# Kernel tuning notes

Measured on AMD Instinct MI355X. Metric: run time of the kernel, lower is better.

The kernel has to match this reference:

```python
import jax, jax.numpy as jnp
import numpy as np

NUM_EMBEDDINGS = 4096
EMBEDDING_DIM = 256
COMMITMENT_COST = 0.25


def setup_inputs() -> dict:
    key = jax.random.key(0)
    k1, k2 = jax.random.split(key)
    x = jax.random.normal(k1, (64, 32, 32, EMBEDDING_DIM), dtype=jnp.float32)
    # torch init: uniform(-1/K, 1/K)
    codebook = jax.random.uniform(
        k2, (NUM_EMBEDDINGS, EMBEDDING_DIM), dtype=jnp.float32,
        minval=-1.0 / NUM_EMBEDDINGS, maxval=1.0 / NUM_EMBEDDINGS)
    return {"x": x, "codebook": codebook}


def reference(x, codebook):
    D = codebook.shape[1]
    flat_x = x.reshape(-1, D)                                   # [N, D]
    distances = (jnp.sum(flat_x ** 2, axis=1, keepdims=True)
                 + jnp.sum(codebook ** 2, axis=1)
                 - 2.0 * flat_x @ codebook.T)                   # [N, K]
    encoding_indices = jnp.argmin(distances, axis=1)            # [N]
    quantized = codebook[encoding_indices].reshape(x.shape)     # gather (== one-hot matmul)
    q_sg = jax.lax.stop_gradient(quantized)
    x_sg = jax.lax.stop_gradient(x)
    commitment_loss = jnp.mean((q_sg - x) ** 2)
    codebook_loss = jnp.mean((quantized - x_sg) ** 2)
    vq_loss = codebook_loss + COMMITMENT_COST * commitment_loss
    # straight-through estimator
    quantized_st = x + jax.lax.stop_gradient(quantized - x)
    return quantized_st, vq_loss
```

## Files before the change

kernel.cpp:

```cpp
#include <hip/hip_runtime.h>
#include <stdint.h>

#define DIM     256
#define NCODES  4096
#define NROWS   65536
#define ROWS_WG 128
#define CCOLS   64
#define NCH     (NCODES / CCOLS)
#define CHB     (CCOLS * DIM)

#define OFF_BIMG  0u
#define OFF_HC    (1u << 20)
#define OFF_PART  ((1u << 20) + 16384u)

typedef __attribute__((ext_vector_type(8)))  int   i32x8;
typedef __attribute__((ext_vector_type(16))) float f32x16;
typedef const __attribute__((address_space(1))) uint32_t* gas1_t;
typedef __attribute__((address_space(3))) uint32_t*       las3_t;

__device__ __forceinline__ uint32_t pk4(float a, float b, float c, float d) {
  uint32_t lo = (uint32_t)__builtin_amdgcn_cvt_pk_fp8_f32(a, b, 0, false) & 0xFFFFu;
  uint32_t hi = (uint32_t)__builtin_amdgcn_cvt_pk_fp8_f32(c, d, 0, false) & 0xFFFFu;
  return lo | (hi << 16);
}

__global__ __launch_bounds__(64) void k1_prep(const float* __restrict__ cb,
                                              uint8_t* __restrict__ ws) {
  const int code = blockIdx.x;
  const int l = threadIdx.x;
  float4 v = ((const float4*)(cb + (size_t)code * DIM))[l];
  float ax = v.x * 4096.0f, ay = v.y * 4096.0f;
  float az = v.z * 4096.0f, aw = v.w * 4096.0f;
  uint32_t off = (uint32_t)(code >> 6) * (uint32_t)CHB
               + (uint32_t)(l >> 2) * 1024u
               + (uint32_t)(code & 63) * 16u + (uint32_t)(l & 3) * 4u;
  *(uint32_t*)(ws + OFF_BIMG + off) = pk4(ax, ay, az, aw);
  float s = ax * ax + ay * ay + az * az + aw * aw;
  #pragma unroll
  for (int m = 1; m < 64; m <<= 1) s += __shfl_xor(s, m, 64);
  if (l == 0) ((float*)(ws + OFF_HC))[code] = 512.0f + s * (1.0f / 8192.0f);
}

__global__ __launch_bounds__(256, 2) void k2_argmin(const float* __restrict__ x,
                                                    const float* __restrict__ cb,
                                                    uint8_t* __restrict__ ws,
                                                    float* __restrict__ out) {
  __shared__ uint4 smem4[2048];
  char* smem = (char*)&smem4[0];
  const int t = threadIdx.x;
  const int wave = t >> 6;
  const int lane = t & 63;
  const int c = lane & 31;
  const int g = lane >> 5;
  const int wg = blockIdx.x;
  const uint8_t* __restrict__ Bimg = ws + OFF_BIMG;
  const float* __restrict__ hcg = (const float*)(ws + OFF_HC);

  const int rbw = (wave >> 1) * 64;
  const int cbw = (wave & 1) * 32;

  const float* xb = x + (size_t)wg * ROWS_WG * DIM;
  {
    #pragma unroll
    for (int it = 0; it < 16; ++it) {
      int u = it * 256 + t;
      int row = u >> 5;
      int k8 = u & 31;
      const float4* src = (const float4*)(xb + (size_t)row * DIM + k8 * 8);
      float4 v0 = src[0], v1 = src[1];
      uint32_t* d = (uint32_t*)(smem + (k8 >> 2) * 4096 + row * 32 + (k8 & 3) * 8);
      d[0] = pk4(-v0.x, -v0.y, -v0.z, -v0.w);
      d[1] = pk4(-v1.x, -v1.y, -v1.z, -v1.w);
    }
  }
  __syncthreads();

  i32x8 a[2][4];
  #pragma unroll
  for (int rt = 0; rt < 2; ++rt)
    #pragma unroll
    for (int ks = 0; ks < 4; ++ks)
      a[rt][ks] = *(const i32x8*)(smem + (ks * 2 + g) * 4096
                                  + (rbw + rt * 32 + c) * 32);
  __syncthreads();

  auto stageB = [&](int buf, int ch) {
    const uint8_t* gsrc = Bimg + (size_t)ch * CHB + (size_t)t * 16;
    char* lb = smem + buf * 16384 + (t & 192) * 16;
    #pragma unroll
    for (int i = 0; i < 4; ++i)
      __builtin_amdgcn_global_load_lds((gas1_t)(uintptr_t)(gsrc + i * 4096),
                                       (las3_t)(uintptr_t)(lb + i * 4096),
                                       16, 0, 0);
  };

  uint32_t key[2][16];
  #pragma unroll
  for (int rt = 0; rt < 2; ++rt)
    #pragma unroll
    for (int r = 0; r < 16; ++r) key[rt][r] = 0xFFFFFFFFu;

  const int hoff = cbw + c;
  const uint32_t maskhi = 0xFFFFF000u;

  const int ch0 = ((wg * 7) + ((wg >> 8) * 29)) & 63;

  stageB(0, ch0);
  float h_cur = hcg[ch0 * CCOLS + hoff];

  for (int i = 0; i < NCH; ++i) {
    const int cur = i & 1;
    const int ch = (ch0 + i) & 63;
    const int chn = (ch0 + i + 1) & 63;
    __syncthreads();
    if (i + 1 < NCH) stageB(cur ^ 1, chn);
    float h_nxt = hcg[chn * CCOLS + hoff];

    f32x16 acc0, acc1;
    #pragma unroll
    for (int j = 0; j < 16; ++j) { acc0[j] = h_cur; acc1[j] = h_cur; }
    const char* bb = smem + cur * 16384 + (cbw + c) * 16;
    #pragma unroll
    for (int ks = 0; ks < 4; ++ks) {
      uint4 b0 = *(const uint4*)(bb + (ks * 4 + g * 2) * 1024);
      uint4 b1 = *(const uint4*)(bb + (ks * 4 + g * 2 + 1) * 1024);
      i32x8 b;
      b[0] = (int)b0.x; b[1] = (int)b0.y; b[2] = (int)b0.z; b[3] = (int)b0.w;
      b[4] = (int)b1.x; b[5] = (int)b1.y; b[6] = (int)b1.z; b[7] = (int)b1.w;
      acc0 = __builtin_amdgcn_mfma_scale_f32_32x32x64_f8f6f4(
                 a[0][ks], b, acc0, 0, 0, 0, 0x7F7F7F7F, 0, 0x7F7F7F7F);
      acc1 = __builtin_amdgcn_mfma_scale_f32_32x32x64_f8f6f4(
                 a[1][ks], b, acc1, 0, 0, 0, 0x7F7F7F7F, 0, 0x7F7F7F7F);
    }
    const uint32_t col = (uint32_t)(ch * CCOLS + hoff);
    #pragma unroll
    for (int r = 0; r < 16; ++r) {
      key[0][r] = min(key[0][r], (__float_as_uint(acc0[r]) & maskhi) | col);
      key[1][r] = min(key[1][r], (__float_as_uint(acc1[r]) & maskhi) | col);
    }
    h_cur = h_nxt;
  }

  #pragma unroll
  for (int rt = 0; rt < 2; ++rt)
    #pragma unroll
    for (int r = 0; r < 16; ++r) {
      uint32_t k = key[rt][r];
      #pragma unroll
      for (int m = 1; m < 32; m <<= 1) {
        uint32_t ko = (uint32_t)__shfl_xor((int)k, m, 32);
        k = min(k, ko);
      }
      key[rt][r] = k;
    }

  uint32_t* bk = (uint32_t*)smem;
  __syncthreads();
  if (t < 128) bk[t] = 0xFFFFFFFFu;
  __syncthreads();
  if (c == 0) {
    #pragma unroll
    for (int rt = 0; rt < 2; ++rt)
      #pragma unroll
      for (int r = 0; r < 16; ++r) {
        int rl = rbw + rt * 32 + (r & 3) + ((r >> 2) << 3) + (g << 2);
        atomicMin(&bk[rl], key[rt][r]);
      }
  }
  __syncthreads();

  float* ob = out + (size_t)wg * ROWS_WG * DIM;
  float psum = 0.0f;
  #pragma unroll 4
  for (int it = 0; it < 32; ++it) {
    int u = it * 256 + t;
    int row = u >> 6;
    int k4i = u & 63;
    int code = (int)(bk[row] & 0xFFFu);
    float4 q = ((const float4*)(cb + (size_t)code * DIM))[k4i];
    float4 xv = ((const float4*)xb)[u];
    ((float4*)ob)[u] = q;
    float dx = q.x - xv.x, dy = q.y - xv.y;
    float dz = q.z - xv.z, dw = q.w - xv.w;
    psum += dx * dx + dy * dy + dz * dz + dw * dw;
  }
  #pragma unroll
  for (int m = 1; m < 64; m <<= 1) psum += __shfl_xor(psum, m, 64);
  __shared__ float ps[4];
  if (lane == 0) ps[wave] = psum;
  __syncthreads();
  if (t == 0)
    ((float*)(ws + OFF_PART))[wg] = ps[0] + ps[1] + ps[2] + ps[3];
}

__global__ __launch_bounds__(256) void k4_loss(const uint8_t* __restrict__ ws,
                                               float* __restrict__ out,
                                               int out_size) {
  const float* part = (const float*)(ws + OFF_PART);
  float s = 0.0f;
  for (int i = threadIdx.x; i < 512; i += 256) s += part[i];
  #pragma unroll
  for (int m = 1; m < 64; m <<= 1) s += __shfl_xor(s, m, 64);
  __shared__ float ps[4];
  if ((threadIdx.x & 63) == 0) ps[threadIdx.x >> 6] = s;
  __syncthreads();
  if (threadIdx.x == 0)
    out[out_size - 1] =
        1.25f * (ps[0] + ps[1] + ps[2] + ps[3]) * (1.0f / 16777216.0f);
}

extern "C" void kernel_launch(void* const* d_in, const int* in_sizes, int n_in,
                              void* d_out, int out_size, void* d_ws, size_t ws_size,
                              hipStream_t stream) {
  const float* x = (const float*)d_in[0];
  const float* cb = (const float*)d_in[1];
  uint8_t* ws = (uint8_t*)d_ws;
  float* out = (float*)d_out;

  k1_prep<<<dim3(NCODES), dim3(64), 0, stream>>>(cb, ws);
  k2_argmin<<<dim3(NROWS / ROWS_WG), dim3(256), 0, stream>>>(x, cb, ws, out);
  k4_loss<<<dim3(1), dim3(256), 0, stream>>>(ws, out, out_size);
}
```

Baseline: 180.5 us.

## Halve rows per workgroup, raise occupancy, and fold loss reduction into atomics

The argmin kernel now handles 64 rows per workgroup instead of 128, with one MFMA tile per wave and launch bounds that ask for 4 workgroups per SIMD group, doubling the grid to 1024 workgroups. The separate loss-reduction kernel is removed: each workgroup atomically adds its scaled partial sum into the output scalar, which the prep kernel zeroes first. The prep kernel also packs four codes per 256-thread block. The aim is more parallelism and latency hiding plus one fewer launch, at the cost of each codebook chunk streamed from L2 being reused by half as many rows, and a loss value that is no longer bit-deterministic.

```diff
diff --git a/kernel.cpp b/kernel.cpp
--- a/kernel.cpp
+++ b/kernel.cpp
@@ -4,14 +4,13 @@
 #define DIM     256
 #define NCODES  4096
 #define NROWS   65536
-#define ROWS_WG 128
+#define ROWS_WG 64
 #define CCOLS   64
 #define NCH     (NCODES / CCOLS)
 #define CHB     (CCOLS * DIM)
 
 #define OFF_BIMG  0u
 #define OFF_HC    (1u << 20)
-#define OFF_PART  ((1u << 20) + 16384u)
 
 typedef __attribute__((ext_vector_type(8)))  int   i32x8;
 typedef __attribute__((ext_vector_type(16))) float f32x16;
@@ -24,10 +23,14 @@
   return lo | (hi << 16);
 }
 
-__global__ __launch_bounds__(64) void k1_prep(const float* __restrict__ cb,
-                                              uint8_t* __restrict__ ws) {
-  const int code = blockIdx.x;
-  const int l = threadIdx.x;
+__global__ __launch_bounds__(256) void k1_prep(const float* __restrict__ cb,
+                                               uint8_t* __restrict__ ws,
+                                               float* __restrict__ out,
+                                               int out_size) {
+  const int t = threadIdx.x;
+  if (blockIdx.x == 0 && t == 0) out[out_size - 1] = 0.0f;
+  const int code = blockIdx.x * 4 + (t >> 6);
+  const int l = t & 63;
   float4 v = ((const float4*)(cb + (size_t)code * DIM))[l];
   float ax = v.x * 4096.0f, ay = v.y * 4096.0f;
   float az = v.z * 4096.0f, aw = v.w * 4096.0f;
@@ -41,10 +44,11 @@
   if (l == 0) ((float*)(ws + OFF_HC))[code] = 512.0f + s * (1.0f / 8192.0f);
 }
 
-__global__ __launch_bounds__(256, 2) void k2_argmin(const float* __restrict__ x,
+__global__ __launch_bounds__(256, 4) void k2_argmin(const float* __restrict__ x,
                                                     const float* __restrict__ cb,
                                                     uint8_t* __restrict__ ws,
-                                                    float* __restrict__ out) {
+                                                    float* __restrict__ out,
+                                                    int out_size) {
   __shared__ uint4 smem4[2048];
   char* smem = (char*)&smem4[0];
   const int t = threadIdx.x;
@@ -56,32 +60,29 @@
   const uint8_t* __restrict__ Bimg = ws + OFF_BIMG;
   const float* __restrict__ hcg = (const float*)(ws + OFF_HC);
 
-  const int rbw = (wave >> 1) * 64;
+  const int rbw = (wave >> 1) * 32;
   const int cbw = (wave & 1) * 32;
 
   const float* xb = x + (size_t)wg * ROWS_WG * DIM;
   {
     #pragma unroll
-    for (int it = 0; it < 16; ++it) {
+    for (int it = 0; it < 8; ++it) {
       int u = it * 256 + t;
       int row = u >> 5;
       int k8 = u & 31;
       const float4* src = (const float4*)(xb + (size_t)row * DIM + k8 * 8);
       float4 v0 = src[0], v1 = src[1];
-      uint32_t* d = (uint32_t*)(smem + (k8 >> 2) * 4096 + row * 32 + (k8 & 3) * 8);
+      uint32_t* d = (uint32_t*)(smem + (k8 >> 2) * 2048 + row * 32 + (k8 & 3) * 8);
       d[0] = pk4(-v0.x, -v0.y, -v0.z, -v0.w);
       d[1] = pk4(-v1.x, -v1.y, -v1.z, -v1.w);
     }
   }
   __syncthreads();
 
-  i32x8 a[2][4];
+  i32x8 a[4];
   #pragma unroll
-  for (int rt = 0; rt < 2; ++rt)
-    #pragma unroll
-    for (int ks = 0; ks < 4; ++ks)
-      a[rt][ks] = *(const i32x8*)(smem + (ks * 2 + g) * 4096
-                                  + (rbw + rt * 32 + c) * 32);
+  for (int ks = 0; ks < 4; ++ks)
+    a[ks] = *(const i32x8*)(smem + (ks * 2 + g) * 2048 + (rbw + c) * 32);
   __syncthreads();
 
   auto stageB = [&](int buf, int ch) {
@@ -94,16 +95,14 @@
                                        16, 0, 0);
   };
 
-  uint32_t key[2][16];
+  uint32_t key[16];
   #pragma unroll
-  for (int rt = 0; rt < 2; ++rt)
-    #pragma unroll
-    for (int r = 0; r < 16; ++r) key[rt][r] = 0xFFFFFFFFu;
+  for (int r = 0; r < 16; ++r) key[r] = 0xFFFFFFFFu;
 
   const int hoff = cbw + c;
   const uint32_t maskhi = 0xFFFFF000u;
 
-  const int ch0 = ((wg * 7) + ((wg >> 8) * 29)) & 63;
+  const int ch0 = ((wg * 7) + ((wg >> 8) * 17)) & 63;
 
   stageB(0, ch0);
   float h_cur = hcg[ch0 * CCOLS + hoff];
@@ -116,9 +115,9 @@
     if (i + 1 < NCH) stageB(cur ^ 1, chn);
     float h_nxt = hcg[chn * CCOLS + hoff];
 
-    f32x16 acc0, acc1;
+    f32x16 acc;
     #pragma unroll
-    for (int j = 0; j < 16; ++j) { acc0[j] = h_cur; acc1[j] = h_cur; }
+    for (int j = 0; j < 16; ++j) acc[j] = h_cur;
     const char* bb = smem + cur * 16384 + (cbw + c) * 16;
     #pragma unroll
     for (int ks = 0; ks < 4; ++ks) {
@@ -127,52 +126,44 @@
       i32x8 b;
       b[0] = (int)b0.x; b[1] = (int)b0.y; b[2] = (int)b0.z; b[3] = (int)b0.w;
       b[4] = (int)b1.x; b[5] = (int)b1.y; b[6] = (int)b1.z; b[7] = (int)b1.w;
-      acc0 = __builtin_amdgcn_mfma_scale_f32_32x32x64_f8f6f4(
-                 a[0][ks], b, acc0, 0, 0, 0, 0x7F7F7F7F, 0, 0x7F7F7F7F);
-      acc1 = __builtin_amdgcn_mfma_scale_f32_32x32x64_f8f6f4(
-                 a[1][ks], b, acc1, 0, 0, 0, 0x7F7F7F7F, 0, 0x7F7F7F7F);
+      acc = __builtin_amdgcn_mfma_scale_f32_32x32x64_f8f6f4(
+                a[ks], b, acc, 0, 0, 0, 0x7F7F7F7F, 0, 0x7F7F7F7F);
     }
     const uint32_t col = (uint32_t)(ch * CCOLS + hoff);
     #pragma unroll
-    for (int r = 0; r < 16; ++r) {
-      key[0][r] = min(key[0][r], (__float_as_uint(acc0[r]) & maskhi) | col);
-      key[1][r] = min(key[1][r], (__float_as_uint(acc1[r]) & maskhi) | col);
-    }
+    for (int r = 0; r < 16; ++r)
+      key[r] = min(key[r], (__float_as_uint(acc[r]) & maskhi) | col);
     h_cur = h_nxt;
   }
 
   #pragma unroll
-  for (int rt = 0; rt < 2; ++rt)
+  for (int r = 0; r < 16; ++r) {
+    uint32_t k = key[r];
     #pragma unroll
-    for (int r = 0; r < 16; ++r) {
-      uint32_t k = key[rt][r];
-      #pragma unroll
-      for (int m = 1; m < 32; m <<= 1) {
-        uint32_t ko = (uint32_t)__shfl_xor((int)k, m, 32);
-        k = min(k, ko);
-      }
-      key[rt][r] = k;
+    for (int m = 1; m < 32; m <<= 1) {
+      uint32_t ko = (uint32_t)__shfl_xor((int)k, m, 32);
+      k = min(k, ko);
     }
+    key[r] = k;
+  }
 
   uint32_t* bk = (uint32_t*)smem;
   __syncthreads();
-  if (t < 128) bk[t] = 0xFFFFFFFFu;
+  if (t < 64) bk[t] = 0xFFFFFFFFu;
   __syncthreads();
   if (c == 0) {
     #pragma unroll
-    for (int rt = 0; rt < 2; ++rt)
-      #pragma unroll
-      for (int r = 0; r < 16; ++r) {
-        int rl = rbw + rt * 32 + (r & 3) + ((r >> 2) << 3) + (g << 2);
-        atomicMin(&bk[rl], key[rt][r]);
-      }
+    for (int r = 0; r < 16; ++r) {
+      int rl = rbw + (r & 3) + ((r >> 2) << 3) + (g << 2);
+      atomicMin(&bk[rl], key[r]);
+    }
   }
   __syncthreads();
 
   float* ob = out + (size_t)wg * ROWS_WG * DIM;
   float psum = 0.0f;
   #pragma unroll 4
-  for (int it = 0; it < 32; ++it) {
+  for (int it = 0; it < 16; ++it) {
     int u = it * 256 + t;
     int row = u >> 6;
     int k4i = u & 63;
@@ -190,23 +181,8 @@
   if (lane == 0) ps[wave] = psum;
   __syncthreads();
   if (t == 0)
-    ((float*)(ws + OFF_PART))[wg] = ps[0] + ps[1] + ps[2] + ps[3];
-}
-
-__global__ __launch_bounds__(256) void k4_loss(const uint8_t* __restrict__ ws,
-                                               float* __restrict__ out,
-                                               int out_size) {
-  const float* part = (const float*)(ws + OFF_PART);
-  float s = 0.0f;
-  for (int i = threadIdx.x; i < 512; i += 256) s += part[i];
-  #pragma unroll
-  for (int m = 1; m < 64; m <<= 1) s += __shfl_xor(s, m, 64);
-  __shared__ float ps[4];
-  if ((threadIdx.x & 63) == 0) ps[threadIdx.x >> 6] = s;
-  __syncthreads();
-  if (threadIdx.x == 0)
-    out[out_size - 1] =
-        1.25f * (ps[0] + ps[1] + ps[2] + ps[3]) * (1.0f / 16777216.0f);
+    atomicAdd(&out[out_size - 1],
+              (ps[0] + ps[1] + ps[2] + ps[3]) * (1.25f / 16777216.0f));
 }
 
 extern "C" void kernel_launch(void* const* d_in, const int* in_sizes, int n_in,
@@ -217,7 +193,6 @@
   uint8_t* ws = (uint8_t*)d_ws;
   float* out = (float*)d_out;
 
-  k1_prep<<<dim3(NCODES), dim3(64), 0, stream>>>(cb, ws);
-  k2_argmin<<<dim3(NROWS / ROWS_WG), dim3(256), 0, stream>>>(x, cb, ws, out);
-  k4_loss<<<dim3(1), dim3(256), 0, stream>>>(ws, out, out_size);
+  k1_prep<<<dim3(NCODES / 4), dim3(256), 0, stream>>>(cb, ws, out, out_size);
+  k2_argmin<<<dim3(NROWS / ROWS_WG), dim3(256), 0, stream>>>(x, cb, ws, out, out_size);
 }
```

Measured after the change: 182.7 us. Within noise of the previous version (+1.2%).

## Load codebook tiles directly into registers and fold loss reduction into atomics

Applied to the files above, without the earlier changes.

The main loop no longer stages codebook fp8 chunks through LDS with global_load_lds and barriers. Each lane now loads its B fragments straight from global memory into registers, double-buffered across two register sets, which removes the per-chunk __syncthreads. The separate loss kernel is dropped: each workgroup atomically adds its scaled partial sum, and the prep kernel zeroes the output slot first. Prep also packs four codes per block. In exchange, every wave now re-reads B from global/L2 instead of sharing one LDS copy, which raises memory traffic and register pressure, and the float atomics make the loss nondeterministic. Chunks are also no longer staggered across workgroups.

```diff
diff --git a/kernel.cpp b/kernel.cpp
--- a/kernel.cpp
+++ b/kernel.cpp
@@ -11,12 +11,9 @@
 
 #define OFF_BIMG  0u
 #define OFF_HC    (1u << 20)
-#define OFF_PART  ((1u << 20) + 16384u)
 
 typedef __attribute__((ext_vector_type(8)))  int   i32x8;
 typedef __attribute__((ext_vector_type(16))) float f32x16;
-typedef const __attribute__((address_space(1))) uint32_t* gas1_t;
-typedef __attribute__((address_space(3))) uint32_t*       las3_t;
 
 __device__ __forceinline__ uint32_t pk4(float a, float b, float c, float d) {
   uint32_t lo = (uint32_t)__builtin_amdgcn_cvt_pk_fp8_f32(a, b, 0, false) & 0xFFFFu;
@@ -24,10 +21,14 @@
   return lo | (hi << 16);
 }
 
-__global__ __launch_bounds__(64) void k1_prep(const float* __restrict__ cb,
-                                              uint8_t* __restrict__ ws) {
-  const int code = blockIdx.x;
-  const int l = threadIdx.x;
+__global__ __launch_bounds__(256) void k1_prep(const float* __restrict__ cb,
+                                               uint8_t* __restrict__ ws,
+                                               float* __restrict__ out,
+                                               int out_size) {
+  const int t = threadIdx.x;
+  if (blockIdx.x == 0 && t == 0) out[out_size - 1] = 0.0f;
+  const int code = blockIdx.x * 4 + (t >> 6);
+  const int l = t & 63;
   float4 v = ((const float4*)(cb + (size_t)code * DIM))[l];
   float ax = v.x * 4096.0f, ay = v.y * 4096.0f;
   float az = v.z * 4096.0f, aw = v.w * 4096.0f;
@@ -44,7 +45,8 @@
 __global__ __launch_bounds__(256, 2) void k2_argmin(const float* __restrict__ x,
                                                     const float* __restrict__ cb,
                                                     uint8_t* __restrict__ ws,
-                                                    float* __restrict__ out) {
+                                                    float* __restrict__ out,
+                                                    int out_size) {
   __shared__ uint4 smem4[2048];
   char* smem = (char*)&smem4[0];
   const int t = threadIdx.x;
@@ -82,17 +84,6 @@
     for (int ks = 0; ks < 4; ++ks)
       a[rt][ks] = *(const i32x8*)(smem + (ks * 2 + g) * 4096
                                   + (rbw + rt * 32 + c) * 32);
-  __syncthreads();
-
-  auto stageB = [&](int buf, int ch) {
-    const uint8_t* gsrc = Bimg + (size_t)ch * CHB + (size_t)t * 16;
-    char* lb = smem + buf * 16384 + (t & 192) * 16;
-    #pragma unroll
-    for (int i = 0; i < 4; ++i)
-      __builtin_amdgcn_global_load_lds((gas1_t)(uintptr_t)(gsrc + i * 4096),
-                                       (las3_t)(uintptr_t)(lb + i * 4096),
-                                       16, 0, 0);
-  };
 
   uint32_t key[2][16];
   #pragma unroll
@@ -103,30 +94,28 @@
   const int hoff = cbw + c;
   const uint32_t maskhi = 0xFFFFF000u;
 
-  const int ch0 = ((wg * 7) + ((wg >> 8) * 29)) & 63;
-
-  stageB(0, ch0);
-  float h_cur = hcg[ch0 * CCOLS + hoff];
-
-  for (int i = 0; i < NCH; ++i) {
-    const int cur = i & 1;
-    const int ch = (ch0 + i) & 63;
-    const int chn = (ch0 + i + 1) & 63;
-    __syncthreads();
-    if (i + 1 < NCH) stageB(cur ^ 1, chn);
-    float h_nxt = hcg[chn * CCOLS + hoff];
-
+  const uint8_t* gbase = Bimg + (size_t)g * 2048 + (size_t)(cbw + c) * 16;
+
+  auto loadB = [&](uint4* dst, int ch) {
+    const uint8_t* gb = gbase + (size_t)ch * CHB;
+    #pragma unroll
+    for (int ks = 0; ks < 4; ++ks) {
+      dst[ks * 2]     = *(const uint4*)(gb + ks * 4096);
+      dst[ks * 2 + 1] = *(const uint4*)(gb + ks * 4096 + 1024);
+    }
+  };
+
+  auto computeC = [&](const uint4* bq, int ch, float h) {
     f32x16 acc0, acc1;
     #pragma unroll
-    for (int j = 0; j < 16; ++j) { acc0[j] = h_cur; acc1[j] = h_cur; }
-    const char* bb = smem + cur * 16384 + (cbw + c) * 16;
+    for (int j = 0; j < 16; ++j) { acc0[j] = h; acc1[j] = h; }
     #pragma unroll
     for (int ks = 0; ks < 4; ++ks) {
-      uint4 b0 = *(const uint4*)(bb + (ks * 4 + g * 2) * 1024);
-      uint4 b1 = *(const uint4*)(bb + (ks * 4 + g * 2 + 1) * 1024);
       i32x8 b;
-      b[0] = (int)b0.x; b[1] = (int)b0.y; b[2] = (int)b0.z; b[3] = (int)b0.w;
-      b[4] = (int)b1.x; b[5] = (int)b1.y; b[6] = (int)b1.z; b[7] = (int)b1.w;
+      b[0] = (int)bq[ks * 2].x;     b[1] = (int)bq[ks * 2].y;
+      b[2] = (int)bq[ks * 2].z;     b[3] = (int)bq[ks * 2].w;
+      b[4] = (int)bq[ks * 2 + 1].x; b[5] = (int)bq[ks * 2 + 1].y;
+      b[6] = (int)bq[ks * 2 + 1].z; b[7] = (int)bq[ks * 2 + 1].w;
       acc0 = __builtin_amdgcn_mfma_scale_f32_32x32x64_f8f6f4(
                  a[0][ks], b, acc0, 0, 0, 0, 0x7F7F7F7F, 0, 0x7F7F7F7F);
       acc1 = __builtin_amdgcn_mfma_scale_f32_32x32x64_f8f6f4(
@@ -138,7 +127,19 @@
       key[0][r] = min(key[0][r], (__float_as_uint(acc0[r]) & maskhi) | col);
       key[1][r] = min(key[1][r], (__float_as_uint(acc1[r]) & maskhi) | col);
     }
-    h_cur = h_nxt;
+  };
+
+  uint4 bA[8], bB[8];
+  float hA, hB;
+  loadB(bA, 0);
+  hA = hcg[hoff];
+  for (int i = 0; i < NCH; i += 2) {
+    loadB(bB, (i + 1) & 63);
+    hB = hcg[((i + 1) & 63) * CCOLS + hoff];
+    computeC(bA, i, hA);
+    loadB(bA, (i + 2) & 63);
+    hA = hcg[((i + 2) & 63) * CCOLS + hoff];
+    computeC(bB, i + 1, hB);
   }
 
   #pragma unroll
@@ -190,23 +191,8 @@
   if (lane == 0) ps[wave] = psum;
   __syncthreads();
   if (t == 0)
-    ((float*)(ws + OFF_PART))[wg] = ps[0] + ps[1] + ps[2] + ps[3];
-}
-
-__global__ __launch_bounds__(256) void k4_loss(const uint8_t* __restrict__ ws,
-                                               float* __restrict__ out,
-                                               int out_size) {
-  const float* part = (const float*)(ws + OFF_PART);
-  float s = 0.0f;
-  for (int i = threadIdx.x; i < 512; i += 256) s += part[i];
-  #pragma unroll
-  for (int m = 1; m < 64; m <<= 1) s += __shfl_xor(s, m, 64);
-  __shared__ float ps[4];
-  if ((threadIdx.x & 63) == 0) ps[threadIdx.x >> 6] = s;
-  __syncthreads();
-  if (threadIdx.x == 0)
-    out[out_size - 1] =
-        1.25f * (ps[0] + ps[1] + ps[2] + ps[3]) * (1.0f / 16777216.0f);
+    atomicAdd(&out[out_size - 1],
+              (ps[0] + ps[1] + ps[2] + ps[3]) * (1.25f / 16777216.0f));
 }
 
 extern "C" void kernel_launch(void* const* d_in, const int* in_sizes, int n_in,
@@ -217,7 +203,6 @@
   uint8_t* ws = (uint8_t*)d_ws;
   float* out = (float*)d_out;
 
-  k1_prep<<<dim3(NCODES), dim3(64), 0, stream>>>(cb, ws);
-  k2_argmin<<<dim3(NROWS / ROWS_WG), dim3(256), 0, stream>>>(x, cb, ws, out);
-  k4_loss<<<dim3(1), dim3(256), 0, stream>>>(ws, out, out_size);
-}
+  k1_prep<<<dim3(NCODES / 4), dim3(256), 0, stream>>>(cb, ws, out, out_size);
+  k2_argmin<<<dim3(NROWS / ROWS_WG), dim3(256), 0, stream>>>(x, cb, ws, out, out_size);
+}
```

After: 189.6 us. 5.0% more time.

## Widen codebook chunks to 128 codes with 8-wave blocks and fuse loss via atomics

Applied to the files above, without the earlier changes.

Doubles the codebook chunk per iteration to 128 columns and the workgroup to 8 waves, so each staged B tile is shared by four column waves and there are half as many chunk iterations and barriers. The prep kernel now packs four codes per block into the new layout and zeroes the loss slot. The separate loss-reduction kernel is removed in favour of a per-block float atomicAdd, saving one launch but making the loss sum order nondeterministic. LDS use doubles to 64KB per block, which may limit how many blocks fit per CU.

```diff
diff --git a/kernel.cpp b/kernel.cpp
--- a/kernel.cpp
+++ b/kernel.cpp
@@ -5,13 +5,12 @@
 #define NCODES  4096
 #define NROWS   65536
 #define ROWS_WG 128
-#define CCOLS   64
+#define CCOLS   128
 #define NCH     (NCODES / CCOLS)
 #define CHB     (CCOLS * DIM)
 
 #define OFF_BIMG  0u
 #define OFF_HC    (1u << 20)
-#define OFF_PART  ((1u << 20) + 16384u)
 
 typedef __attribute__((ext_vector_type(8)))  int   i32x8;
 typedef __attribute__((ext_vector_type(16))) float f32x16;
@@ -24,16 +23,20 @@
   return lo | (hi << 16);
 }
 
-__global__ __launch_bounds__(64) void k1_prep(const float* __restrict__ cb,
-                                              uint8_t* __restrict__ ws) {
-  const int code = blockIdx.x;
-  const int l = threadIdx.x;
+__global__ __launch_bounds__(256) void k1_prep(const float* __restrict__ cb,
+                                               uint8_t* __restrict__ ws,
+                                               float* __restrict__ out,
+                                               int out_size) {
+  const int t = threadIdx.x;
+  if (blockIdx.x == 0 && t == 0) out[out_size - 1] = 0.0f;
+  const int code = blockIdx.x * 4 + (t >> 6);
+  const int l = t & 63;
   float4 v = ((const float4*)(cb + (size_t)code * DIM))[l];
   float ax = v.x * 4096.0f, ay = v.y * 4096.0f;
   float az = v.z * 4096.0f, aw = v.w * 4096.0f;
-  uint32_t off = (uint32_t)(code >> 6) * (uint32_t)CHB
-               + (uint32_t)(l >> 2) * 1024u
-               + (uint32_t)(code & 63) * 16u + (uint32_t)(l & 3) * 4u;
+  uint32_t off = (uint32_t)(code >> 7) * (uint32_t)CHB
+               + (uint32_t)(l >> 2) * 2048u
+               + (uint32_t)(code & 127) * 16u + (uint32_t)(l & 3) * 4u;
   *(uint32_t*)(ws + OFF_BIMG + off) = pk4(ax, ay, az, aw);
   float s = ax * ax + ay * ay + az * az + aw * aw;
   #pragma unroll
@@ -41,11 +44,12 @@
   if (l == 0) ((float*)(ws + OFF_HC))[code] = 512.0f + s * (1.0f / 8192.0f);
 }
 
-__global__ __launch_bounds__(256, 2) void k2_argmin(const float* __restrict__ x,
+__global__ __launch_bounds__(512, 4) void k2_argmin(const float* __restrict__ x,
                                                     const float* __restrict__ cb,
                                                     uint8_t* __restrict__ ws,
-                                                    float* __restrict__ out) {
-  __shared__ uint4 smem4[2048];
+                                                    float* __restrict__ out,
+                                                    int out_size) {
+  __shared__ uint4 smem4[4096];
   char* smem = (char*)&smem4[0];
   const int t = threadIdx.x;
   const int wave = t >> 6;
@@ -56,14 +60,14 @@
   const uint8_t* __restrict__ Bimg = ws + OFF_BIMG;
   const float* __restrict__ hcg = (const float*)(ws + OFF_HC);
 
-  const int rbw = (wave >> 1) * 64;
-  const int cbw = (wave & 1) * 32;
+  const int rbw = (wave >> 2) * 64;
+  const int cbw = (wave & 3) * 32;
 
   const float* xb = x + (size_t)wg * ROWS_WG * DIM;
   {
     #pragma unroll
-    for (int it = 0; it < 16; ++it) {
-      int u = it * 256 + t;
+    for (int it = 0; it < 8; ++it) {
+      int u = it * 512 + t;
       int row = u >> 5;
       int k8 = u & 31;
       const float4* src = (const float4*)(xb + (size_t)row * DIM + k8 * 8);
@@ -86,11 +90,11 @@
 
   auto stageB = [&](int buf, int ch) {
     const uint8_t* gsrc = Bimg + (size_t)ch * CHB + (size_t)t * 16;
-    char* lb = smem + buf * 16384 + (t & 192) * 16;
+    char* lb = smem + buf * 32768 + (t & 448) * 16;
     #pragma unroll
     for (int i = 0; i < 4; ++i)
-      __builtin_amdgcn_global_load_lds((gas1_t)(uintptr_t)(gsrc + i * 4096),
-                                       (las3_t)(uintptr_t)(lb + i * 4096),
+      __builtin_amdgcn_global_load_lds((gas1_t)(uintptr_t)(gsrc + i * 8192),
+                                       (las3_t)(uintptr_t)(lb + i * 8192),
                                        16, 0, 0);
   };
 
@@ -103,15 +107,15 @@
   const int hoff = cbw + c;
   const uint32_t maskhi = 0xFFFFF000u;
 
-  const int ch0 = ((wg * 7) + ((wg >> 8) * 29)) & 63;
+  const int ch0 = ((wg * 7) + ((wg >> 8) * 13)) & 31;
 
   stageB(0, ch0);
   float h_cur = hcg[ch0 * CCOLS + hoff];
 
   for (int i = 0; i < NCH; ++i) {
     const int cur = i & 1;
-    const int ch = (ch0 + i) & 63;
-    const int chn = (ch0 + i + 1) & 63;
+    const int ch = (ch0 + i) & 31;
+    const int chn = (ch0 + i + 1) & 31;
     __syncthreads();
     if (i + 1 < NCH) stageB(cur ^ 1, chn);
     float h_nxt = hcg[chn * CCOLS + hoff];
@@ -119,11 +123,11 @@
     f32x16 acc0, acc1;
     #pragma unroll
     for (int j = 0; j < 16; ++j) { acc0[j] = h_cur; acc1[j] = h_cur; }
-    const char* bb = smem + cur * 16384 + (cbw + c) * 16;
+    const char* bb = smem + cur * 32768 + (cbw + c) * 16;
     #pragma unroll
     for (int ks = 0; ks < 4; ++ks) {
-      uint4 b0 = *(const uint4*)(bb + (ks * 4 + g * 2) * 1024);
-      uint4 b1 = *(const uint4*)(bb + (ks * 4 + g * 2 + 1) * 1024);
+      uint4 b0 = *(const uint4*)(bb + (ks * 4 + g * 2) * 2048);
+      uint4 b1 = *(const uint4*)(bb + (ks * 4 + g * 2 + 1) * 2048);
       i32x8 b;
       b[0] = (int)b0.x; b[1] = (int)b0.y; b[2] = (int)b0.z; b[3] = (int)b0.w;
       b[4] = (int)b1.x; b[5] = (int)b1.y; b[6] = (int)b1.z; b[7] = (int)b1.w;
@@ -172,8 +176,8 @@
   float* ob = out + (size_t)wg * ROWS_WG * DIM;
   float psum = 0.0f;
   #pragma unroll 4
-  for (int it = 0; it < 32; ++it) {
-    int u = it * 256 + t;
+  for (int it = 0; it < 16; ++it) {
+    int u = it * 512 + t;
     int row = u >> 6;
     int k4i = u & 63;
     int code = (int)(bk[row] & 0xFFFu);
@@ -186,27 +190,15 @@
   }
   #pragma unroll
   for (int m = 1; m < 64; m <<= 1) psum += __shfl_xor(psum, m, 64);
-  __shared__ float ps[4];
+  __shared__ float ps[8];
   if (lane == 0) ps[wave] = psum;
   __syncthreads();
-  if (t == 0)
-    ((float*)(ws + OFF_PART))[wg] = ps[0] + ps[1] + ps[2] + ps[3];
-}
-
-__global__ __launch_bounds__(256) void k4_loss(const uint8_t* __restrict__ ws,
-                                               float* __restrict__ out,
-                                               int out_size) {
-  const float* part = (const float*)(ws + OFF_PART);
-  float s = 0.0f;
-  for (int i = threadIdx.x; i < 512; i += 256) s += part[i];
-  #pragma unroll
-  for (int m = 1; m < 64; m <<= 1) s += __shfl_xor(s, m, 64);
-  __shared__ float ps[4];
-  if ((threadIdx.x & 63) == 0) ps[threadIdx.x >> 6] = s;
-  __syncthreads();
-  if (threadIdx.x == 0)
-    out[out_size - 1] =
-        1.25f * (ps[0] + ps[1] + ps[2] + ps[3]) * (1.0f / 16777216.0f);
+  if (t == 0) {
+    float s = 0.0f;
+    #pragma unroll
+    for (int w = 0; w < 8; ++w) s += ps[w];
+    atomicAdd(&out[out_size - 1], s * (1.25f / 16777216.0f));
+  }
 }
 
 extern "C" void kernel_launch(void* const* d_in, const int* in_sizes, int n_in,
@@ -217,7 +209,6 @@
   uint8_t* ws = (uint8_t*)d_ws;
   float* out = (float*)d_out;
 
-  k1_prep<<<dim3(NCODES), dim3(64), 0, stream>>>(cb, ws);
-  k2_argmin<<<dim3(NROWS / ROWS_WG), dim3(256), 0, stream>>>(x, cb, ws, out);
-  k4_loss<<<dim3(1), dim3(256), 0, stream>>>(ws, out, out_size);
-}
+  k1_prep<<<dim3(NCODES / 4), dim3(256), 0, stream>>>(cb, ws, out, out_size);
+  k2_argmin<<<dim3(NROWS / ROWS_WG), dim3(512), 0, stream>>>(x, cb, ws, out, out_size);
+}
```

Result: slower. 254.2 us (+40.8%).
